# Optimization experiments

Measured on AMD Instinct MI355X. Metric: run time of the kernel, lower is better.

The kernel has to match this reference:

```python
import jax, jax.numpy as jnp
import numpy as np

DN = ('NCHW', 'OIHW', 'NCHW')

def _conv(x, w, groups=1, padding=0):
    return jax.lax.conv_general_dilated(
        x, w, window_strides=(1, 1), padding=[(padding, padding)] * 2,
        dimension_numbers=DN, feature_group_count=groups)

def _bn(x, scale, shift):
    # precomputed inference BN: x * scale + shift, per channel (NCHW)
    return x * scale[None, :, None, None] + shift[None, :, None, None]

def _channel_shuffle(x, g):
    n, c, h, w = x.shape
    return x.reshape(n, g, c // g, h, w).transpose(0, 2, 1, 3, 4).reshape(n, c, h, w)

def setup_inputs() -> dict:
    key = jax.random.key(0)
    ks = jax.random.split(key, 13)
    N, Cin, H, W = 32, 240, 56, 56
    Cout, G = 480, 3
    mid = Cout // 4  # 120
    inp = {
        'x': jax.random.normal(ks[0], (N, Cin, H, W), jnp.float32),
        'w1': jax.random.normal(ks[1], (mid, Cin // G, 1, 1), jnp.float32) * 0.05,
        'scale1': jax.random.uniform(ks[2], (mid,), jnp.float32, 0.5, 1.5),
        'shift1': jax.random.normal(ks[3], (mid,), jnp.float32) * 0.1,
        'w2': jax.random.normal(ks[4], (mid, 1, 3, 3), jnp.float32) * 0.05,
        'scale2': jax.random.uniform(ks[5], (mid,), jnp.float32, 0.5, 1.5),
        'shift2': jax.random.normal(ks[6], (mid,), jnp.float32) * 0.1,
        'w3': jax.random.normal(ks[7], (Cout, mid // G, 1, 1), jnp.float32) * 0.05,
        'scale3': jax.random.uniform(ks[8], (Cout,), jnp.float32, 0.5, 1.5),
        'shift3': jax.random.normal(ks[9], (Cout,), jnp.float32) * 0.1,
        'wsc': jax.random.normal(ks[10], (Cout, Cin, 1, 1), jnp.float32) * 0.05,
        'scale_sc': jax.random.uniform(ks[11], (Cout,), jnp.float32, 0.5, 1.5),
        'shift_sc': jax.random.normal(ks[12], (Cout,), jnp.float32) * 0.1,
        'groups': G,
    }
    return inp

def reference(x, w1, scale1, shift1, w2, scale2, shift2, w3, scale3, shift3,
              wsc, scale_sc, shift_sc, groups):
    g = int(groups)
    mid = w1.shape[0]
    # conv1 (grouped 1x1) -> fused BN + ReLU
    y = _conv(x, w1, groups=g)
    y = jax.nn.relu(_bn(y, scale1, shift1))
    # conv2 (depthwise 3x3) -> fused BN + channel shuffle
    y = _conv(y, w2, groups=mid, padding=1)
    y = _channel_shuffle(_bn(y, scale2, shift2), g)
    # conv3 (grouped 1x1)
    y = _conv(y, w3, groups=g)
    # shortcut: 1x1 conv (in_channels != out_channels)
    z = _conv(x, wsc)
    # fused final: relu(BN3(y)) + BN_sc(z)
    return jax.nn.relu(_bn(y, scale3, shift3)) + _bn(z, scale_sc, shift_sc)
```

## Files before the change

### kernel.cpp

```cpp
#include <hip/hip_runtime.h>

typedef short bf16x8 __attribute__((ext_vector_type(8)));
typedef float f32x4 __attribute__((ext_vector_type(4)));

namespace {
constexpr int kHW = 3136;
constexpr int kNPx = 32 * kHW;
constexpr int kPtiles = kNPx / 16;
constexpr size_t kXbiShorts = (size_t)kPtiles * 4096;
constexpr size_t kY2iShorts = (size_t)kPtiles * 2048;
}

__device__ __align__(16) unsigned short g_w1i[3 * 4 * 48 * 32];
__device__ __align__(16) unsigned short g_wsci[8 * 480 * 32];
__device__ __align__(16) unsigned short g_w3i[2 * 480 * 32];
__device__ __align__(16) float g_w2f[9 * 120];

static __device__ __forceinline__ unsigned short f2b(float f) {
  unsigned u = __float_as_uint(f);
  u = (u + 0x7fffu + ((u >> 16) & 1u)) >> 16;
  return (unsigned short)u;
}
static __device__ __forceinline__ float b2f(unsigned short u) {
  return __uint_as_float((unsigned)u << 16);
}
static __device__ __forceinline__ f32x4 mfma16(bf16x8 a, bf16x8 b, f32x4 c) {
  return __builtin_amdgcn_mfma_f32_16x16x32_bf16(a, b, c, 0, 0, 0);
}
static __device__ __forceinline__ bf16x8 ldg8(const unsigned short* p) {
  return *reinterpret_cast<const bf16x8*>(p);
}

__global__ __launch_bounds__(256) void prep_weights(
    const float* __restrict__ w1, const float* __restrict__ wsc,
    const float* __restrict__ w3, const float* __restrict__ w2,
    const float* __restrict__ scale2) {
  const int idx = blockIdx.x * 256 + threadIdx.x;
  if (idx < 18432) {
    const int g = idx / 6144, r = idx % 6144, kb = r / 1536;
    const int j = (r % 1536) / 32, k = r % 32;
    const int gk = g * 64 + kb * 32 + k;
    const int c = gk - g * 80;
    unsigned short v = 0;
    if (j < 40 && c >= 0 && c < 80) v = f2b(w1[(g * 40 + j) * 80 + c]);
    g_w1i[idx] = v;
  } else if (idx < 18432 + 122880) {
    const int i = idx - 18432;
    const int kb = i / 15360, co = (i % 15360) / 32, k = i % 32;
    const int c = kb * 32 + k;
    g_wsci[i] = (c < 240) ? f2b(wsc[co * 240 + c]) : (unsigned short)0;
  } else if (idx < 18432 + 122880 + 30720) {
    const int i = idx - 141312;
    const int kb = i / 15360, co = (i % 15360) / 32, k = i % 32;
    const int cb = co / 160;
    const int s = cb * 32 + kb * 32 + k - cb * 40;
    g_w3i[i] = (s >= 0 && s < 40) ? f2b(w3[co * 40 + s]) : (unsigned short)0;
  } else if (idx < 18432 + 122880 + 30720 + 1080) {
    const int i = idx - 172032;
    const int tap = i / 120, c = i % 120;
    g_w2f[i] = w2[c * 9 + tap] * scale2[c];
  }
}

__global__ __launch_bounds__(256) void transpose_interleave(
    const float* __restrict__ x, unsigned short* __restrict__ xbi) {
  const int P0 = blockIdx.x * 64;
  const int px_loc = threadIdx.x >> 2, part = threadIdx.x & 3;
  const int P = P0 + px_loc;
  const int n = P / kHW, hw = P % kHW;
  const int pt = px_loc >> 4, l = px_loc & 15;
  unsigned short* dst =
      xbi + ((size_t)(P0 / 16) + pt) * 4096 + l * 32 + part * 8;
  const float* xp = x + ((size_t)n * 240) * kHW + hw;
#pragma unroll
  for (int kb = 0; kb < 8; ++kb) {
    unsigned short v[8];
#pragma unroll
    for (int j = 0; j < 8; ++j) {
      const int c = kb * 32 + part * 8 + j;
      v[j] = (c < 240) ? f2b(xp[(size_t)c * kHW]) : (unsigned short)0;
    }
    *reinterpret_cast<uint4*>(dst + kb * 512) =
        *reinterpret_cast<const uint4*>(v);
  }
}

__global__ __launch_bounds__(256) void conv1_gemm(
    const unsigned short* __restrict__ xbi, const float* __restrict__ scale1,
    const float* __restrict__ shift1, unsigned short* __restrict__ y1) {
  const int lane = threadIdx.x & 63;
  const int wv = threadIdx.x >> 6;
  const int l15 = lane & 15, quad = lane >> 4;
  const size_t PT = (size_t)blockIdx.x * 8 + wv * 2;

#pragma unroll
  for (int g = 0; g < 3; ++g) {
    f32x4 acc[2][3];
#pragma unroll
    for (int mt = 0; mt < 2; ++mt)
#pragma unroll
      for (int nt = 0; nt < 3; ++nt) acc[mt][nt] = (f32x4){0.f, 0.f, 0.f, 0.f};
#pragma unroll
    for (int kb = 0; kb < 4; ++kb) {
      const int kbi = 2 * g + kb;
      bf16x8 A[2];
#pragma unroll
      for (int mt = 0; mt < 2; ++mt)
        A[mt] = ldg8(xbi + (PT + mt) * 4096 + kbi * 512 + l15 * 32 + quad * 8);
#pragma unroll
      for (int nt = 0; nt < 3; ++nt) {
        const bf16x8 B = ldg8(g_w1i + (((g * 4 + kb) * 48) + nt * 16 + l15) * 32 +
                              quad * 8);
#pragma unroll
        for (int mt = 0; mt < 2; ++mt) acc[mt][nt] = mfma16(A[mt], B, acc[mt][nt]);
      }
    }
#pragma unroll
    for (int nt = 0; nt < 3; ++nt) {
      const int j = nt * 16 + l15;
      if (j < 40) {
        const int c = g * 40 + j;
        const float sc = scale1[c], sh = shift1[c];
#pragma unroll
        for (int mt = 0; mt < 2; ++mt) {
          const size_t pxb = (PT + mt) * 16 + quad * 4;
#pragma unroll
          for (int r = 0; r < 4; ++r) {
            float v = fmaf(acc[mt][nt][r], sc, sh);
            v = v > 0.f ? v : 0.f;
            y1[(pxb + r) * 120 + c] = f2b(v);
          }
        }
      }
    }
  }
}

__global__ __launch_bounds__(256) void dw_shuffle(
    const unsigned short* __restrict__ y1, const float* __restrict__ shift2,
    unsigned short* __restrict__ y2i) {
  const int pt = blockIdx.x;
  const int t = threadIdx.x;
  __shared__ float lds_y2[16 * 121];

  if (t < 240) {
    const int px_l = t / 15, m = t % 15;
    const int c0 = m * 8;
    const int px = pt * 16 + px_l;
    const int n = px / kHW, hw = px % kHW;
    const int h = hw / 56, w = hw % 56;

    float acc[8];
    {
      const float4 s0 = *reinterpret_cast<const float4*>(shift2 + c0);
      const float4 s1 = *reinterpret_cast<const float4*>(shift2 + c0 + 4);
      acc[0] = s0.x; acc[1] = s0.y; acc[2] = s0.z; acc[3] = s0.w;
      acc[4] = s1.x; acc[5] = s1.y; acc[6] = s1.z; acc[7] = s1.w;
    }
    const unsigned short* yb = y1 + (size_t)n * kHW * 120 + c0;
#pragma unroll
    for (int dy = 0; dy < 3; ++dy) {
      const int hh = h + dy - 1;
      if (hh >= 0 && hh < 56) {
#pragma unroll
        for (int dx = 0; dx < 3; ++dx) {
          const int ww = w + dx - 1;
          if (ww >= 0 && ww < 56) {
            const bf16x8 v = ldg8(yb + (size_t)(hh * 56 + ww) * 120);
            const float* wp = g_w2f + (dy * 3 + dx) * 120 + c0;
            float wv_[8];
            *reinterpret_cast<float4*>(wv_) =
                *reinterpret_cast<const float4*>(wp);
            *reinterpret_cast<float4*>(wv_ + 4) =
                *reinterpret_cast<const float4*>(wp + 4);
#pragma unroll
            for (int j = 0; j < 8; ++j)
              acc[j] = fmaf(b2f((unsigned short)v[j]), wv_[j], acc[j]);
          }
        }
      }
    }
#pragma unroll
    for (int j = 0; j < 8; ++j) lds_y2[px_l * 121 + c0 + j] = acc[j];
  }
  __syncthreads();

  const int q = t * 8;
  const int kb = q >> 9, r = q & 511, pxl = r >> 5, k0 = r & 31;
  unsigned short v[8];
#pragma unroll
  for (int j = 0; j < 8; ++j) {
    const int cn = kb * 32 + k0 + j;
    const int c = (cn % 3) * 40 + cn / 3;
    v[j] = (cn < 120) ? f2b(lds_y2[pxl * 121 + c]) : (unsigned short)0;
  }
  *reinterpret_cast<uint4*>(y2i + (size_t)pt * 2048 + q) =
      *reinterpret_cast<const uint4*>(v);
}

__global__ __launch_bounds__(256, 3) void conv3_sc_gemm(
    const unsigned short* __restrict__ xbi,
    const unsigned short* __restrict__ y2i, const float* __restrict__ scale3,
    const float* __restrict__ shift3, const float* __restrict__ ssc,
    const float* __restrict__ bsc, float* __restrict__ out) {
  const int bid = blockIdx.x;
  const int l = (bid & 7) * 294 + (bid >> 3);
  const int pxb = l / 3;
  const int cb = l % 3;
  const int P0 = pxb * 128;
  const int lane = threadIdx.x & 63;
  const int wv = threadIdx.x >> 6;
  const int mh = wv & 1, nh = wv >> 1;
  const int l15 = lane & 15, quad = lane >> 4;
  const int cbase = cb * 160 + nh * 80;

  f32x4 acc[4][5];
#pragma unroll
  for (int mt = 0; mt < 4; ++mt)
#pragma unroll
    for (int nt = 0; nt < 5; ++nt) acc[mt][nt] = (f32x4){0.f, 0.f, 0.f, 0.f};

  const size_t PT = (size_t)(P0 / 16) + mh * 4;

#pragma unroll
  for (int kb = 0; kb < 2; ++kb) {
    const int kbi = cb + kb;
    bf16x8 A[4];
#pragma unroll
    for (int mt = 0; mt < 4; ++mt)
      A[mt] = ldg8(y2i + (PT + mt) * 2048 + kbi * 512 + l15 * 32 + quad * 8);
#pragma unroll
    for (int nt = 0; nt < 5; ++nt) {
      const bf16x8 B =
          ldg8(g_w3i + ((kb * 480) + cbase + nt * 16 + l15) * 32 + quad * 8);
#pragma unroll
      for (int mt = 0; mt < 4; ++mt) acc[mt][nt] = mfma16(A[mt], B, acc[mt][nt]);
    }
  }

#pragma unroll
  for (int nt = 0; nt < 5; ++nt) {
    const int co = cbase + nt * 16 + l15;
    const float s3 = scale3[co], h3 = shift3[co];
    const float is = 1.0f / ssc[co], h_ = bsc[co];
#pragma unroll
    for (int mt = 0; mt < 4; ++mt)
#pragma unroll
      for (int r = 0; r < 4; ++r) {
        float v3 = fmaf(acc[mt][nt][r], s3, h3);
        v3 = v3 > 0.f ? v3 : 0.f;
        acc[mt][nt][r] = (v3 + h_) * is;
      }
  }

  for (int kb = 0; kb < 8; ++kb) {
    bf16x8 A[4];
#pragma unroll
    for (int mt = 0; mt < 4; ++mt)
      A[mt] = ldg8(xbi + (PT + mt) * 4096 + kb * 512 + l15 * 32 + quad * 8);
#pragma unroll
    for (int nt = 0; nt < 5; ++nt) {
      const bf16x8 B =
          ldg8(g_wsci + ((kb * 480) + cbase + nt * 16 + l15) * 32 + quad * 8);
#pragma unroll
      for (int mt = 0; mt < 4; ++mt) acc[mt][nt] = mfma16(A[mt], B, acc[mt][nt]);
    }
  }

#pragma unroll
  for (int mt = 0; mt < 4; ++mt) {
    const int P = P0 + mh * 64 + mt * 16 + quad * 4;
    const int n = P / kHW, hw = P % kHW;
    float* ob = out + (size_t)n * 480 * kHW + hw;
#pragma unroll
    for (int nt = 0; nt < 5; ++nt) {
      const int co = cbase + nt * 16 + l15;
      const float s_ = ssc[co];
      float4 r;
      float* rp = reinterpret_cast<float*>(&r);
#pragma unroll
      for (int r4 = 0; r4 < 4; ++r4) rp[r4] = s_ * acc[mt][nt][r4];
      *reinterpret_cast<float4*>(ob + (size_t)co * kHW) = r;
    }
  }
}

extern "C" void kernel_launch(void* const* d_in, const int* in_sizes, int n_in,
                              void* d_out, int out_size, void* d_ws,
                              size_t ws_size, hipStream_t stream) {
  const float* x = (const float*)d_in[0];
  const float* w1 = (const float*)d_in[1];
  const float* scale1 = (const float*)d_in[2];
  const float* shift1 = (const float*)d_in[3];
  const float* w2 = (const float*)d_in[4];
  const float* scale2 = (const float*)d_in[5];
  const float* shift2 = (const float*)d_in[6];
  const float* w3 = (const float*)d_in[7];
  const float* scale3 = (const float*)d_in[8];
  const float* shift3 = (const float*)d_in[9];
  const float* wsc = (const float*)d_in[10];
  const float* ssc = (const float*)d_in[11];
  const float* bsc = (const float*)d_in[12];
  float* out = (float*)d_out;

  unsigned short* xbi = (unsigned short*)d_ws;
  unsigned short* y2i = xbi + kXbiShorts;
  unsigned short* y1 = y2i + kY2iShorts;

  prep_weights<<<677, 256, 0, stream>>>(w1, wsc, w3, w2, scale2);
  transpose_interleave<<<kNPx / 64, 256, 0, stream>>>(x, xbi);
  conv1_gemm<<<kPtiles / 8, 256, 0, stream>>>(xbi, scale1, shift1, y1);
  dw_shuffle<<<kPtiles, 256, 0, stream>>>(y1, shift2, y2i);
  conv3_sc_gemm<<<784 * 3, 256, 0, stream>>>(xbi, y2i, scale3, shift3, ssc,
                                             bsc, out);
}
```

Measured before the change: 431.6 us.

## Fuse input transpose with conv1 GEMM and use nontemporal loads/stores

Merges the transpose/bf16-interleave kernel with the grouped conv1 GEMM. Each wave keeps its packed bf16 pixel tile in registers and feeds it straight into the MFMAs, so conv1 no longer re-reads xbi from global memory and one launch goes away. Loads of x, the xbi store and the final output store are now nontemporal to reduce cache pollution. In exchange each wave handles a single M-tile, so there is less B-operand reuse per weight load and register pressure goes up.

```diff
diff --git a/kernel.cpp b/kernel.cpp
--- a/kernel.cpp
+++ b/kernel.cpp
@@ -2,6 +2,7 @@
 
 typedef short bf16x8 __attribute__((ext_vector_type(8)));
 typedef float f32x4 __attribute__((ext_vector_type(4)));
+typedef unsigned int u32x4 __attribute__((ext_vector_type(4)));
 
 namespace {
 constexpr int kHW = 3136;
@@ -62,57 +63,50 @@
   }
 }
 
-__global__ __launch_bounds__(256) void transpose_interleave(
-    const float* __restrict__ x, unsigned short* __restrict__ xbi) {
+__global__ __launch_bounds__(256) void t_conv1(
+    const float* __restrict__ x, const float* __restrict__ scale1,
+    const float* __restrict__ shift1, unsigned short* __restrict__ xbi,
+    unsigned short* __restrict__ y1) {
   const int P0 = blockIdx.x * 64;
-  const int px_loc = threadIdx.x >> 2, part = threadIdx.x & 3;
-  const int P = P0 + px_loc;
-  const int n = P / kHW, hw = P % kHW;
-  const int pt = px_loc >> 4, l = px_loc & 15;
-  unsigned short* dst =
-      xbi + ((size_t)(P0 / 16) + pt) * 4096 + l * 32 + part * 8;
-  const float* xp = x + ((size_t)n * 240) * kHW + hw;
+  const int lane = threadIdx.x & 63;
+  const int wv = threadIdx.x >> 6;
+  const int l15 = lane & 15, part = lane >> 4;
+  const size_t PT = (size_t)(P0 / 16) + wv;
+  const int px = P0 + wv * 16 + l15;
+  const int n = px / kHW, hw = px % kHW;
+
+  bf16x8 pk[8];
+  const float* xp = x + (size_t)n * 240 * kHW + hw;
+  unsigned short* gdst = xbi + PT * 4096 + l15 * 32 + part * 8;
 #pragma unroll
   for (int kb = 0; kb < 8; ++kb) {
-    unsigned short v[8];
+    bf16x8 t;
 #pragma unroll
     for (int j = 0; j < 8; ++j) {
       const int c = kb * 32 + part * 8 + j;
-      v[j] = (c < 240) ? f2b(xp[(size_t)c * kHW]) : (unsigned short)0;
-    }
-    *reinterpret_cast<uint4*>(dst + kb * 512) =
-        *reinterpret_cast<const uint4*>(v);
-  }
-}
-
-__global__ __launch_bounds__(256) void conv1_gemm(
-    const unsigned short* __restrict__ xbi, const float* __restrict__ scale1,
-    const float* __restrict__ shift1, unsigned short* __restrict__ y1) {
-  const int lane = threadIdx.x & 63;
-  const int wv = threadIdx.x >> 6;
-  const int l15 = lane & 15, quad = lane >> 4;
-  const size_t PT = (size_t)blockIdx.x * 8 + wv * 2;
-
+      t[j] = (c < 240)
+                 ? (short)f2b(__builtin_nontemporal_load(xp + (size_t)c * kHW))
+                 : (short)0;
+    }
+    pk[kb] = t;
+    __builtin_nontemporal_store(__builtin_bit_cast(u32x4, t),
+                                reinterpret_cast<u32x4*>(gdst + kb * 512));
+  }
+
+  const int quad = part;
 #pragma unroll
   for (int g = 0; g < 3; ++g) {
-    f32x4 acc[2][3];
-#pragma unroll
-    for (int mt = 0; mt < 2; ++mt)
-#pragma unroll
-      for (int nt = 0; nt < 3; ++nt) acc[mt][nt] = (f32x4){0.f, 0.f, 0.f, 0.f};
+    f32x4 acc[3];
+#pragma unroll
+    for (int nt = 0; nt < 3; ++nt) acc[nt] = (f32x4){0.f, 0.f, 0.f, 0.f};
 #pragma unroll
     for (int kb = 0; kb < 4; ++kb) {
-      const int kbi = 2 * g + kb;
-      bf16x8 A[2];
-#pragma unroll
-      for (int mt = 0; mt < 2; ++mt)
-        A[mt] = ldg8(xbi + (PT + mt) * 4096 + kbi * 512 + l15 * 32 + quad * 8);
+      const bf16x8 A = pk[2 * g + kb];
 #pragma unroll
       for (int nt = 0; nt < 3; ++nt) {
         const bf16x8 B = ldg8(g_w1i + (((g * 4 + kb) * 48) + nt * 16 + l15) * 32 +
                               quad * 8);
-#pragma unroll
-        for (int mt = 0; mt < 2; ++mt) acc[mt][nt] = mfma16(A[mt], B, acc[mt][nt]);
+        acc[nt] = mfma16(A, B, acc[nt]);
       }
     }
 #pragma unroll
@@ -121,15 +115,12 @@
       if (j < 40) {
         const int c = g * 40 + j;
         const float sc = scale1[c], sh = shift1[c];
-#pragma unroll
-        for (int mt = 0; mt < 2; ++mt) {
-          const size_t pxb = (PT + mt) * 16 + quad * 4;
-#pragma unroll
-          for (int r = 0; r < 4; ++r) {
-            float v = fmaf(acc[mt][nt][r], sc, sh);
-            v = v > 0.f ? v : 0.f;
-            y1[(pxb + r) * 120 + c] = f2b(v);
-          }
+        const size_t pxb = PT * 16 + quad * 4;
+#pragma unroll
+        for (int r = 0; r < 4; ++r) {
+          float v = fmaf(acc[nt][r], sc, sh);
+          v = v > 0.f ? v : 0.f;
+          y1[(pxb + r) * 120 + c] = f2b(v);
         }
       }
     }
@@ -276,11 +267,11 @@
     for (int nt = 0; nt < 5; ++nt) {
       const int co = cbase + nt * 16 + l15;
       const float s_ = ssc[co];
-      float4 r;
-      float* rp = reinterpret_cast<float*>(&r);
-#pragma unroll
-      for (int r4 = 0; r4 < 4; ++r4) rp[r4] = s_ * acc[mt][nt][r4];
-      *reinterpret_cast<float4*>(ob + (size_t)co * kHW) = r;
+      f32x4 r;
+#pragma unroll
+      for (int r4 = 0; r4 < 4; ++r4) r[r4] = s_ * acc[mt][nt][r4];
+      __builtin_nontemporal_store(
+          r, reinterpret_cast<f32x4*>(ob + (size_t)co * kHW));
     }
   }
 }
@@ -308,8 +299,7 @@
   unsigned short* y1 = y2i + kY2iShorts;
 
   prep_weights<<<677, 256, 0, stream>>>(w1, wsc, w3, w2, scale2);
-  transpose_interleave<<<kNPx / 64, 256, 0, stream>>>(x, xbi);
-  conv1_gemm<<<kPtiles / 8, 256, 0, stream>>>(xbi, scale1, shift1, y1);
+  t_conv1<<<kNPx / 64, 256, 0, stream>>>(x, scale1, shift1, xbi, y1);
   dw_shuffle<<<kPtiles, 256, 0, stream>>>(y1, shift2, y2i);
   conv3_sc_gemm<<<784 * 3, 256, 0, stream>>>(xbi, y2i, scale3, shift3, ssc,
                                              bsc, out);
```

New measurement: 432.7 us. No clear change (+0.3%).
